# Kernel tuning notes

Hardware: AMD Instinct MI355X
Metric: run time of the kernel (lower is better)

Reference implementation:

```python
import jax, jax.numpy as jnp
import numpy as np

B, C, E, T, K = 8, 256, 512, 8192, 512
BN_EPS = 1e-5
UN_EPS = 1e-8


def setup_inputs() -> dict:
    key = jax.random.key(0)
    ks = jax.random.split(key, 6)
    sc_up = 1.0 / np.sqrt(C)
    sc_lin = 1.0 / np.sqrt(E)
    return {
        "x": jax.random.normal(ks[0], (B, C, T), jnp.float32),
        "up_w": jax.random.normal(ks[1], (E, C), jnp.float32) * sc_up,
        "up_b": jnp.zeros((E,), jnp.float32),
        "mask_w": jax.random.normal(ks[2], (E, C), jnp.float32) * sc_up,
        "mask_b": jnp.zeros((E,), jnp.float32),
        "sum_w": jax.random.normal(ks[3], (C, E), jnp.float32) * sc_lin,
        "sum_b": jnp.zeros((C,), jnp.float32),
        "down_w": jax.random.normal(ks[4], (C, E), jnp.float32) * sc_lin,
        "down_b": jnp.zeros((C,), jnp.float32),
        "bn_w": jnp.ones((C,), jnp.float32),
        "bn_b": jnp.zeros((C,), jnp.float32),
    }


def reference(x, up_w, up_b, mask_w, mask_b, sum_w, sum_b, down_w, down_b, bn_w, bn_b):
    b = x.shape[0]
    orig = x
    # 1x1 conv = channel matmul: (E,C) x (b,C,T) -> (b,E,T)
    up = jnp.einsum("ec,bct->bet", up_w, x) + up_b[None, :, None]
    # unit_norm over channel dim
    un = orig / (jnp.linalg.norm(orig, axis=1, keepdims=True) + UN_EPS)
    m = jnp.einsum("ec,bct->bet", mask_w, un) + mask_b[None, :, None]
    # softmax over flattened (E*T) per batch
    sm = jax.nn.softmax(m.reshape(b, -1), axis=-1)
    # sparsify: keep top-K softmax values per batch, zero the rest
    vals, idx = jax.lax.top_k(sm, K)  # (b,K)
    sp = jnp.zeros_like(sm).at[jnp.arange(b)[:, None], idx].set(vals)
    sp = sp.reshape(up.shape)
    gated = sp * up  # (b,E,T)
    summary = jnp.sum(gated, axis=-1)  # (b,E)
    proj = summary @ sum_w.T + sum_b  # (b,C)
    down = jnp.einsum("ce,bet->bct", down_w, gated) + down_b[None, :, None]
    y = down + proj[:, :, None]
    # BatchNorm1d (training mode: batch statistics, biased variance)
    mean = jnp.mean(y, axis=(0, 2), keepdims=True)
    var = jnp.var(y, axis=(0, 2), keepdims=True)
    out = (y - mean) / jnp.sqrt(var + BN_EPS) * bn_w[None, :, None] + bn_b[None, :, None]
    return out
```

## Files before the change

### kernel.cpp

```cpp
#include <hip/hip_runtime.h>
#include <hip/hip_bf16.h>

#define B_ 8
#define C_ 256
#define E_ 512
#define T_ 8192
#define K_ 512
#define CT_ (C_*T_)
#define BCAP_ 512
#define OCAP_ 1024
#define NBLK_ 2048
#define SUBS_ 64
#define SCOLS_ (T_/SUBS_)
#define SUBN_ (E_*SCOLS_)
#define RANK_ 64
#define NB1_ 4096
#define NB2_ 4096
#define TAUP_ 8
#define TAUM_ 0.004f

typedef __attribute__((ext_vector_type(8))) short bf16x8;
typedef __attribute__((ext_vector_type(4))) float f32x4;

__device__ __forceinline__ ushort f2bf(float f) {
    __hip_bfloat16 h = __float2bfloat16(f);
    return *reinterpret_cast<ushort*>(&h);
}
__device__ __forceinline__ float bf2f(ushort u) {
    __hip_bfloat16 h = *reinterpret_cast<__hip_bfloat16*>(&u);
    return __bfloat162float(h);
}

__device__ __forceinline__ void gl16(const void* g, void* l) {
    __builtin_amdgcn_global_load_lds(
        (const __attribute__((address_space(1))) void*)g,
        (__attribute__((address_space(3))) void*)l, 16, 0, 0);
}


__launch_bounds__(256)
__global__ void k_rn(const float* __restrict__ x, float* __restrict__ rn,
                     float* __restrict__ nrm, int* __restrict__ ovc,
                     int* __restrict__ map, float* __restrict__ spk) {
    __shared__ float partial[4][64];
    int tid = threadIdx.x, lane = tid & 63, w = tid >> 6;
    int bid = blockIdx.x;
    int gid = bid * 256 + tid;
    if (gid < B_) ovc[gid] = 0;
    if (gid < B_ * T_) map[gid] = -1;
    ((float4*)spk)[gid] = (float4){0.f, 0.f, 0.f, 0.f};
    int b = bid >> 7;
    int t = (bid & 127) * 64 + lane;
    const float* xp = x + (size_t)b * CT_ + (size_t)(w * 64) * T_ + t;
    float s0 = 0.f, s1 = 0.f, s2 = 0.f, s3 = 0.f;
#pragma unroll 4
    for (int c = 0; c < 64; c += 4) {
        float a0 = xp[(size_t)c * T_];
        float a1 = xp[(size_t)(c + 1) * T_];
        float a2 = xp[(size_t)(c + 2) * T_];
        float a3 = xp[(size_t)(c + 3) * T_];
        s0 += a0 * a0; s1 += a1 * a1; s2 += a2 * a2; s3 += a3 * a3;
    }
    partial[w][lane] = (s0 + s1) + (s2 + s3);
    __syncthreads();
    if (w == 0) {
        float s = (partial[0][lane] + partial[1][lane])
                + (partial[2][lane] + partial[3][lane]);
        float n = sqrtf(s) + 1e-8f;
        nrm[b * T_ + t] = n;
        rn[b * T_ + t] = 1.0f / n;
    }
}

__global__ void k_split_w(const float* __restrict__ mw, ushort* __restrict__ mwh,
                          ushort* __restrict__ mwl) {
    int idx = blockIdx.x * 256 + threadIdx.x;
    int erow = idx & 63;
    int cb = (idx >> 6) & 7;
    int cc = (idx >> 9) & 3;
    int etile = idx >> 11;
    int e = etile * 64 + erow;
    int c0 = cc * 64 + cb * 8;
    const float* src = mw + (size_t)e * C_ + c0;
    ushort4 h0, l0, h1, l1;
    float v;
    v = src[0]; h0.x = f2bf(v); l0.x = f2bf(v - bf2f(h0.x));
    v = src[1]; h0.y = f2bf(v); l0.y = f2bf(v - bf2f(h0.y));
    v = src[2]; h0.z = f2bf(v); l0.z = f2bf(v - bf2f(h0.z));
    v = src[3]; h0.w = f2bf(v); l0.w = f2bf(v - bf2f(h0.w));
    v = src[4]; h1.x = f2bf(v); l1.x = f2bf(v - bf2f(h1.x));
    v = src[5]; h1.y = f2bf(v); l1.y = f2bf(v - bf2f(h1.y));
    v = src[6]; h1.z = f2bf(v); l1.z = f2bf(v - bf2f(h1.z));
    v = src[7]; h1.w = f2bf(v); l1.w = f2bf(v - bf2f(h1.w));
    *(ushort4*)(mwh + (size_t)idx * 8) = h0;
    *(ushort4*)(mwh + (size_t)idx * 8 + 4) = h1;
    *(ushort4*)(mwl + (size_t)idx * 8) = l0;
    *(ushort4*)(mwl + (size_t)idx * 8 + 4) = l1;
}

__launch_bounds__(256)
__global__ void k_split_x(const float* __restrict__ x, const float* __restrict__ rn,
                          ushort* __restrict__ xh, ushort* __restrict__ xl) {
    __shared__ float tile[64][76];
    __shared__ float rnv[64];
    int tid = threadIdx.x;
    int ttile = blockIdx.x, cc = blockIdx.y, b = blockIdx.z;
    int t0 = ttile * 64, c0 = cc * 64;
    if (tid < 64) rnv[tid] = rn[b * T_ + t0 + tid];
    const float* xb = x + (size_t)b * CT_;
#pragma unroll
    for (int q = 0; q < 4; ++q) {
        int idx = tid + q * 256;
        int cr = idx >> 4, t4 = (idx & 15) * 4;
        float4 v = *(const float4*)(xb + (size_t)(c0 + cr) * T_ + t0 + t4);
        *(float4*)&tile[cr][t4] = v;
    }
    __syncthreads();
    size_t obase = (((size_t)b * 128 + ttile) * 4 + cc) * 4096;
#pragma unroll
    for (int q = 0; q < 4; ++q) {
        int idx = tid + q * 256;
        int tr = idx >> 4, c4 = (idx & 15) * 4;
        float s = rnv[tr];
        float v0 = tile[c4 + 0][tr] * s;
        float v1 = tile[c4 + 1][tr] * s;
        float v2 = tile[c4 + 2][tr] * s;
        float v3 = tile[c4 + 3][tr] * s;
        ushort4 h, l;
        h.x = f2bf(v0); l.x = f2bf(v0 - bf2f(h.x));
        h.y = f2bf(v1); l.y = f2bf(v1 - bf2f(h.y));
        h.z = f2bf(v2); l.z = f2bf(v2 - bf2f(h.z));
        h.w = f2bf(v3); l.w = f2bf(v3 - bf2f(h.w));
        int cb = c4 >> 3, half = (c4 >> 2) & 1;
        size_t ro = obase + (size_t)cb * 512 + tr * 8 + half * 4;
        *(ushort4*)(xh + ro) = h;
        *(ushort4*)(xl + ro) = l;
    }
}

__global__ void k_gather(const float* __restrict__ x, const float* __restrict__ rn,
                         float* __restrict__ xs, int* __restrict__ gh) {
    int gid = blockIdx.x * 256 + threadIdx.x;
    if (gid < B_ * NB1_) gh[gid] = 0;
    int s = gid & (SCOLS_ - 1);
    int c = (gid >> 7) & (C_ - 1);
    int b = gid >> 15;
    int t = s * SUBS_;
    xs[gid] = x[(size_t)b * CT_ + (size_t)c * T_ + t] * rn[b * T_ + t];
}

__launch_bounds__(256)
__global__ void k_msub2(const float* __restrict__ xs, const float* __restrict__ mw,
                        const float* __restrict__ mb, float* __restrict__ msub) {
    __shared__ float As[64][68];
    __shared__ float Bs[64][68];
    int tid = threadIdx.x;
    int tx = tid & 15, ty = tid >> 4;
    int s0 = blockIdx.x * 64, e0 = blockIdx.y * 64, b = blockIdx.z;
    const float* xb = xs + (size_t)b * C_ * SCOLS_;
    float acc[4][4] = {};
    for (int c0 = 0; c0 < C_; c0 += 64) {
#pragma unroll
        for (int r = 0; r < 4; ++r) {
            int i = (tid >> 4) + r * 16;
            int kq = (tid & 15) * 4;
            float4 av = *(const float4*)(mw + (size_t)(e0 + i) * C_ + c0 + kq);
            As[kq + 0][i] = av.x; As[kq + 1][i] = av.y;
            As[kq + 2][i] = av.z; As[kq + 3][i] = av.w;
        }
#pragma unroll
        for (int r = 0; r < 4; ++r) {
            int k = (tid >> 4) + r * 16;
            int jq = (tid & 15) * 4;
            *(float4*)(&Bs[k][jq]) =
                *(const float4*)(xb + (size_t)(c0 + k) * SCOLS_ + s0 + jq);
        }
        __syncthreads();
#pragma unroll
        for (int k = 0; k < 64; ++k) {
            float4 a = *(const float4*)(&As[k][ty * 4]);
            float4 bq = *(const float4*)(&Bs[k][tx * 4]);
            float av[4] = {a.x, a.y, a.z, a.w};
            float bv[4] = {bq.x, bq.y, bq.z, bq.w};
#pragma unroll
            for (int ii = 0; ii < 4; ++ii)
#pragma unroll
                for (int jj = 0; jj < 4; ++jj)
                    acc[ii][jj] += av[ii] * bv[jj];
        }
        __syncthreads();
    }
#pragma unroll
    for (int ii = 0; ii < 4; ++ii) {
        float mbv = mb[e0 + ty * 4 + ii];
#pragma unroll
        for (int jj = 0; jj < 4; ++jj) {
            int e = e0 + ty * 4 + ii, s = s0 + tx * 4 + jj;
            msub[(size_t)b * SUBN_ + e * SCOLS_ + s] = acc[ii][jj] + mbv;
        }
    }
}

__launch_bounds__(256)
__global__ void k_tau_hist(const float* __restrict__ msub, int* __restrict__ gh) {
    __shared__ int h[NB1_];
    int tid = threadIdx.x;
    int b = blockIdx.x >> 3, part = blockIdx.x & (TAUP_ - 1);
    for (int i = tid; i < NB1_; i += 256) h[i] = 0;
    __syncthreads();
    const float* mp = msub + (size_t)b * SUBN_ + part * (SUBN_ / TAUP_);
    for (int j = tid; j < SUBN_ / TAUP_; j += 256) {
        float v = mp[j];
        int bin = (int)((v + 1.0f) * ((float)NB1_ * 0.5f));
        bin = bin < 0 ? 0 : (bin > NB1_ - 1 ? NB1_ - 1 : bin);
        atomicAdd(&h[bin], 1);
    }
    __syncthreads();
    int* ghb = gh + b * NB1_;
    for (int i = tid; i < NB1_; i += 256)
        if (h[i]) atomicAdd(&ghb[i], h[i]);
}

__global__ void k_tau2(const int* __restrict__ gh, float* __restrict__ tau0) {
    __shared__ int part[256];
    int b = blockIdx.x, tid = threadIdx.x;
    const int* h = gh + b * NB1_;
    int ps = 0;
    for (int j = 0; j < 16; ++j) ps += h[tid * 16 + j];
    part[tid] = ps;
    __syncthreads();
    if (tid == 0) {
        int cum = 0, bf = 0;
        for (int i = 255; i >= 0; --i) {
            if (cum + part[i] >= RANK_) {
                int cum2 = cum;
                for (int j = 15; j >= 0; --j) {
                    cum2 += h[i * 16 + j];
                    if (cum2 >= RANK_) { bf = i * 16 + j; break; }
                }
                break;
            }
            cum += part[i];
        }
        tau0[b] = (float)bf * (2.0f / (float)NB1_) - 1.0f;
    }
}

__launch_bounds__(256)
__global__ void k_gemm128(const ushort* __restrict__ mwh, const ushort* __restrict__ xh,
                          const float* __restrict__ mb, const float* __restrict__ tau0,
                          float* __restrict__ zpart, int* __restrict__ cntB,
                          float* __restrict__ cvalB, int* __restrict__ cidxB,
                          int* __restrict__ ovc, float* __restrict__ ovv,
                          int* __restrict__ ovi) {
    __shared__ ushort S[4][4096];
    __shared__ float red[4];
    __shared__ float sval[BCAP_];
    __shared__ int sidx[BCAP_];
    __shared__ int scnt;
    int tid = threadIdx.x, lane = tid & 63, w = tid >> 6;
    int f = blockIdx.x;
    int xcd = f & 7, slot = f >> 3;
    int eblk = slot & 3, xt = slot >> 2;
    int xtile = xcd * 64 + xt;
    int b = xtile >> 6, tt = xtile & 63;
    int e0 = eblk * 128, t0 = tt * 128;
    if (tid == 0) scnt = 0;

    const ushort* base;
    if (w < 2) base = mwh + (size_t)(eblk * 2 + (w & 1)) * 16384;
    else       base = xh + ((size_t)b * 128 + tt * 2 + (w & 1)) * 16384;
    const ushort* gsrc = base + lane * 8;

    f32x4 acc[4][4];
#pragma unroll
    for (int m = 0; m < 4; ++m)
#pragma unroll
        for (int n = 0; n < 4; ++n)
            acc[m][n] = (f32x4){0.f, 0.f, 0.f, 0.f};

    int a15 = lane & 15;
    int khalf = lane >> 4;
    int wr = w >> 1, wc = w & 1;

    for (int cc = 0; cc < 4; ++cc) {
#pragma unroll
        for (int i = 0; i < 8; ++i)
            gl16(gsrc + cc * 4096 + i * 512, &S[w][0] + i * 512);
        __syncthreads();
#pragma unroll
        for (int ks = 0; ks < 2; ++ks) {
            int cb16 = ks * 4 + khalf;
            bf16x8 ah[4], bh[4];
#pragma unroll
            for (int m = 0; m < 4; ++m) {
                int aoff = (cb16 * 64 + m * 16 + a15) * 16;
                ah[m] = *(const bf16x8*)((const char*)&S[wr][0] + aoff);
            }
#pragma unroll
            for (int n = 0; n < 4; ++n) {
                int boff = (cb16 * 64 + n * 16 + a15) * 16;
                bh[n] = *(const bf16x8*)((const char*)&S[2 + wc][0] + boff);
            }
#pragma unroll
            for (int m = 0; m < 4; ++m)
#pragma unroll
                for (int n = 0; n < 4; ++n)
                    acc[m][n] = __builtin_amdgcn_mfma_f32_16x16x32_bf16(ah[m], bh[n], acc[m][n], 0, 0, 0);
        }
        __syncthreads();
    }

    float tau = tau0[b] - TAUM_;
    float zs = 0.f;
    int erow0 = e0 + wr * 64 + (lane >> 4) * 4;
#pragma unroll
    for (int m = 0; m < 4; ++m)
#pragma unroll
        for (int r = 0; r < 4; ++r) {
            int e = erow0 + m * 16 + r;
            float mbe = mb[e];
#pragma unroll
            for (int n = 0; n < 4; ++n) {
                int t = t0 + wc * 64 + n * 16 + a15;
                float v = acc[m][n][r] + mbe;
                zs += __expf(v);
                if (v >= tau) {
                    int pos = atomicAdd(&scnt, 1);
                    if (pos < BCAP_) {
                        sval[pos] = v;
                        sidx[pos] = e * T_ + t;
                    } else {
                        int q2 = atomicAdd(&ovc[b], 1);
                        if (q2 < OCAP_) {
                            ovv[b * OCAP_ + q2] = v;
                            ovi[b * OCAP_ + q2] = e * T_ + t;
                        }
                    }
                }
            }
        }
#pragma unroll
    for (int off = 32; off; off >>= 1) zs += __shfl_xor(zs, off, 64);
    if (lane == 0) red[w] = zs;
    __syncthreads();
    int nc = scnt < BCAP_ ? scnt : BCAP_;
    for (int j = tid; j < nc; j += 256) {
        cvalB[(size_t)f * BCAP_ + j] = sval[j];
        cidxB[(size_t)f * BCAP_ + j] = sidx[j];
    }
    if (tid == 0) {
        cntB[f] = nc;
        zpart[f] = (red[0] + red[1]) + (red[2] + red[3]);
    }
}

__launch_bounds__(256)
__global__ void k_exact(const ushort* __restrict__ mwh, const ushort* __restrict__ mwl,
                        const ushort* __restrict__ xh, const ushort* __restrict__ xl,
                        const float* __restrict__ mb, const int* __restrict__ cntB,
                        const int* __restrict__ cidxB, float* __restrict__ cvalB,
                        const int* __restrict__ ovc, const int* __restrict__ ovi,
                        float* __restrict__ ovv) {
    int f = blockIdx.x;
    int wv = threadIdx.x >> 6, lane = threadIdx.x & 63;
    int cc = lane >> 4, cb = (lane >> 1) & 7, half = lane & 1;
    int n, b;
    const int* ip;
    float* vp;
    if (f < NBLK_) {
        b = f & 7;
        n = cntB[f]; if (n > BCAP_) n = BCAP_;
        ip = cidxB + (size_t)f * BCAP_;
        vp = cvalB + (size_t)f * BCAP_;
    } else {
        b = f - NBLK_;
        n = ovc[b]; if (n > OCAP_) n = OCAP_;
        ip = ovi + (size_t)b * OCAP_;
        vp = ovv + (size_t)b * OCAP_;
    }
    for (int j = wv; j < n; j += 4) {
        int idx = ip[j];
        int e = idx >> 13, t = idx & (T_ - 1);
        size_t xro = ((((size_t)b * 128 + (t >> 6)) * 4 + cc) * 8 + cb) * 512
                   + (size_t)(t & 63) * 8 + half * 4;
        size_t wro = (((size_t)(e >> 6) * 4 + cc) * 8 + cb) * 512
                   + (size_t)(e & 63) * 8 + half * 4;
        ushort4 hx = *(const ushort4*)(xh + xro);
        ushort4 lx = *(const ushort4*)(xl + xro);
        ushort4 hw = *(const ushort4*)(mwh + wro);
        ushort4 lw = *(const ushort4*)(mwl + wro);
        float a = (bf2f(hw.x) + bf2f(lw.x)) * (bf2f(hx.x) + bf2f(lx.x))
                + (bf2f(hw.y) + bf2f(lw.y)) * (bf2f(hx.y) + bf2f(lx.y))
                + (bf2f(hw.z) + bf2f(lw.z)) * (bf2f(hx.z) + bf2f(lx.z))
                + (bf2f(hw.w) + bf2f(lw.w)) * (bf2f(hx.w) + bf2f(lx.w));
#pragma unroll
        for (int off = 32; off; off >>= 1) a += __shfl_xor(a, off, 64);
        if (lane == 0) vp[j] = a + mb[e];
    }
}

__launch_bounds__(1024)
__global__ void k_selectc(const float* __restrict__ zpart, const int* __restrict__ cntB,
                          const float* __restrict__ cvalB, const int* __restrict__ cidxB,
                          const int* __restrict__ ovc, const float* __restrict__ ovv,
                          const int* __restrict__ ovi, int* __restrict__ sel_e,
                          int* __restrict__ sel_t, float* __restrict__ sel_sp) {
    __shared__ float zsh[256];
    __shared__ int h[NB2_];
    __shared__ int part[256];
    __shared__ float bl_v[1024];
    __shared__ int bl_i[1024];
    __shared__ int nb, bstar, nabove, outcnt;
    int b = blockIdx.x, tid = threadIdx.x;
    int rid = tid & 255, sub = tid >> 8;
    int f = b + 8 * rid;
    int c = cntB[f];
    for (int i = tid; i < NB2_; i += 1024) h[i] = 0;
    if (tid < 256) zsh[tid] = zpart[b + 8 * tid];
    if (tid == 0) { nb = 0; outcnt = 0; bstar = 0; nabove = 0; }
    __syncthreads();
    const float* rv = cvalB + (size_t)f * BCAP_;
    for (int j = sub; j < c; j += 4) {
        float v = rv[j];
        int bin = (int)(v * ((float)NB2_ * 2.0f));
        bin = bin < 0 ? 0 : (bin > NB2_ - 1 ? NB2_ - 1 : bin);
        atomicAdd(&h[bin], 1);
    }
    int no = ovc[b]; if (no > OCAP_) no = OCAP_;
    for (int j = tid; j < no; j += 1024) {
        float v = ovv[b * OCAP_ + j];
        int bin = (int)(v * ((float)NB2_ * 2.0f));
        bin = bin < 0 ? 0 : (bin > NB2_ - 1 ? NB2_ - 1 : bin);
        atomicAdd(&h[bin], 1);
    }
    __syncthreads();
    for (int d = 128; d; d >>= 1) {
        if (tid < d) zsh[tid] += zsh[tid + d];
        __syncthreads();
    }
    if (tid < 256) {
        int ps = 0;
#pragma unroll
        for (int j = 0; j < 16; ++j) ps += h[tid * 16 + j];
        part[tid] = ps;
    }
    __syncthreads();
    for (int d = 1; d < 256; d <<= 1) {
        int v = 0;
        if (tid < 256) v = (tid + d < 256) ? part[tid + d] : 0;
        __syncthreads();
        if (tid < 256) part[tid] += v;
        __syncthreads();
    }
    if (tid < 256 && part[tid] >= K_ && (tid == 255 || part[tid + 1] < K_)) {
        int cum2 = (tid == 255) ? 0 : part[tid + 1];
        for (int j = 15; j >= 0; --j) {
            cum2 += h[tid * 16 + j];
            if (cum2 >= K_) { bstar = tid * 16 + j; nabove = cum2 - h[tid * 16 + j]; break; }
        }
    }
    __syncthreads();
    int bs = bstar;
    float rZ = 1.0f / zsh[0];
    const int* ri = cidxB + (size_t)f * BCAP_;
    for (int j = sub; j < c; j += 4) {
        float v = rv[j];
        int bin = (int)(v * ((float)NB2_ * 2.0f));
        bin = bin < 0 ? 0 : (bin > NB2_ - 1 ? NB2_ - 1 : bin);
        if (bin > bs) {
            int q = atomicAdd(&outcnt, 1);
            int idx = ri[j];
            sel_e[b * K_ + q] = idx / T_;
            sel_t[b * K_ + q] = idx % T_;
            sel_sp[b * K_ + q] = __expf(v) * rZ;
        } else if (bin == bs) {
            int q = atomicAdd(&nb, 1);
            if (q < 1024) { bl_v[q] = v; bl_i[q] = ri[j]; }
        }
    }
    for (int j = tid; j < no; j += 1024) {
        float v = ovv[b * OCAP_ + j];
        int bin = (int)(v * ((float)NB2_ * 2.0f));
        bin = bin < 0 ? 0 : (bin > NB2_ - 1 ? NB2_ - 1 : bin);
        if (bin > bs) {
            int q = atomicAdd(&outcnt, 1);
            int idx = ovi[b * OCAP_ + j];
            sel_e[b * K_ + q] = idx / T_;
            sel_t[b * K_ + q] = idx % T_;
            sel_sp[b * K_ + q] = __expf(v) * rZ;
        } else if (bin == bs) {
            int q = atomicAdd(&nb, 1);
            if (q < 1024) { bl_v[q] = v; bl_i[q] = ovi[b * OCAP_ + j]; }
        }
    }
    __syncthreads();
    int m = nb; if (m > 1024) m = 1024;
    int need = K_ - nabove;
    for (int j = tid; j < m; j += 1024) {
        float v = bl_v[j]; int id = bl_i[j];
        int r = 0;
        for (int i = 0; i < m; ++i) {
            float vi = bl_v[i]; int ii = bl_i[i];
            r += (vi > v || (vi == v && ii < id)) ? 1 : 0;
        }
        if (r < need) {
            int slot = nabove + r;
            sel_e[b * K_ + slot] = id / T_;
            sel_t[b * K_ + slot] = id % T_;
            sel_sp[b * K_ + slot] = __expf(v) * rZ;
        }
    }
    for (int q = m + tid; q < need; q += 1024) {
        int slot = nabove + q;
        sel_e[b * K_ + slot] = 0; sel_t[b * K_ + slot] = 0;
        sel_sp[b * K_ + slot] = 0.f;
    }
}

__global__ void k_upg2(const ushort* __restrict__ xh, const ushort* __restrict__ xl,
                       const float* __restrict__ nrm, const float* __restrict__ uw,
                       const float* __restrict__ ub, const int* __restrict__ sel_e,
                       const int* __restrict__ sel_t, const float* __restrict__ sel_sp,
                       float* __restrict__ gval) {
    int gid = blockIdx.x * 256 + threadIdx.x;
    int w = gid >> 6, lane = gid & 63;
    int b = w >> 9, i = w & (K_ - 1);
    int e = sel_e[b * K_ + i], t = sel_t[b * K_ + i];
    int ttile = t >> 6, trow = t & 63;
    int cc = lane >> 4, cb = (lane >> 1) & 7, half = lane & 1;
    size_t ro = ((((size_t)b * 128 + ttile) * 4 + cc) * 8 + cb) * 512
              + (size_t)trow * 8 + half * 4;
    ushort4 h = *(const ushort4*)(xh + ro);
    ushort4 l = *(const ushort4*)(xl + ro);
    float4 wv = *(const float4*)(uw + (size_t)e * C_ + lane * 4);
    float acc = (bf2f(h.x) + bf2f(l.x)) * wv.x + (bf2f(h.y) + bf2f(l.y)) * wv.y
              + (bf2f(h.z) + bf2f(l.z)) * wv.z + (bf2f(h.w) + bf2f(l.w)) * wv.w;
#pragma unroll
    for (int off = 32; off; off >>= 1) acc += __shfl_down(acc, off, 64);
    if (lane == 0)
        gval[b * K_ + i] = sel_sp[b * K_ + i] * (acc * nrm[b * T_ + t] + ub[e]);
}

__launch_bounds__(256)
__global__ void k_bsqbn(const float* __restrict__ sw, const float* __restrict__ sb,
                        const float* __restrict__ db, const float* __restrict__ dw,
                        const int* __restrict__ sel_e, const float* __restrict__ gval,
                        const float* __restrict__ bnw, const float* __restrict__ bnb,
                        float* __restrict__ scalec, float* __restrict__ obase) {
    __shared__ float barr[8], s1arr[8], qarr[8];
    int c = blockIdx.x;
    int w = threadIdx.x >> 6, lane = threadIdx.x & 63;
#pragma unroll
    for (int rep = 0; rep < 2; ++rep) {
        int b = w + rep * 4;
        float p = 0.f, s = 0.f, q = 0.f;
        for (int i = lane; i < K_; i += 64) {
            int e = sel_e[b * K_ + i];
            float g = gval[b * K_ + i];
            p += g * sw[(size_t)c * E_ + e];
            float wv = dw[(size_t)c * E_ + e] * g;
            s += wv; q += wv * wv;
        }
#pragma unroll
        for (int off = 32; off; off >>= 1) {
            p += __shfl_xor(p, off, 64);
            s += __shfl_xor(s, off, 64);
            q += __shfl_xor(q, off, 64);
        }
        if (lane == 0) {
            barr[b] = p + sb[c] + db[c];
            s1arr[b] = s; qarr[b] = q;
        }
    }
    __syncthreads();
    if (threadIdx.x == 0) {
        float msum = 0.f;
        for (int b = 0; b < B_; ++b) msum += (float)T_ * barr[b] + s1arr[b];
        float mean = msum / (float)(B_ * T_);
        float vs = 0.f;
        for (int b = 0; b < B_; ++b) {
            float d = barr[b] - mean;
            vs += (float)T_ * d * d + 2.0f * d * s1arr[b] + qarr[b];
        }
        float var = vs / (float)(B_ * T_);
        float sc = bnw[c] * rsqrtf(var + 1e-5f);
        scalec[c] = sc;
        for (int b = 0; b < B_; ++b)
            obase[b * C_ + c] = (barr[b] - mean) * sc + bnb[c];
    }
}

__global__ void k_spk1(const int* __restrict__ sel_t, int* __restrict__ map,
                       int* __restrict__ pri) {
    int gid = blockIdx.x * 256 + threadIdx.x;
    int b = gid >> 9;
    int t = sel_t[gid];
    int old = atomicCAS(&map[b * T_ + t], -1, gid & (K_ - 1));
    pri[gid] = (old == -1) ? (gid & (K_ - 1)) : old;
}

__global__ void k_spk2(const float* __restrict__ dw, const float* __restrict__ scalec,
                       const int* __restrict__ sel_e, const int* __restrict__ pri,
                       const float* __restrict__ gval, float* __restrict__ spk) {
    int gid = blockIdx.x * 256 + threadIdx.x;
    int s = gid >> 6, cq = (gid & 63) * 4;
    int b = s >> 9;
    int e = sel_e[s];
    float g = gval[s];
    int p = pri[s];
    float* dst = spk + ((size_t)(b * K_ + p)) * C_ + cq;
#pragma unroll
    for (int q = 0; q < 4; ++q) {
        int c = cq + q;
        atomicAdd(dst + q, scalec[c] * dw[(size_t)c * E_ + e] * g);
    }
}

__global__ void k_fill2(const float* __restrict__ obase, const int* __restrict__ map,
                        const float* __restrict__ spk, float* __restrict__ out) {
    size_t gid = (size_t)blockIdx.x * 256 + threadIdx.x;
    size_t flat = gid * 4;
    int b = (int)(flat / CT_);
    int c = (int)(flat / T_) & (C_ - 1);
    int t0 = (int)(flat & (T_ - 1));
    float v = obase[b * C_ + c];
    float4 o = {v, v, v, v};
    int4 mp = *(const int4*)(map + b * T_ + t0);
    if (mp.x >= 0) o.x += spk[((size_t)(b * K_ + mp.x)) * C_ + c];
    if (mp.y >= 0) o.y += spk[((size_t)(b * K_ + mp.y)) * C_ + c];
    if (mp.z >= 0) o.z += spk[((size_t)(b * K_ + mp.z)) * C_ + c];
    if (mp.w >= 0) o.w += spk[((size_t)(b * K_ + mp.w)) * C_ + c];
    *(float4*)(out + flat) = o;
}

extern "C" void kernel_launch(void* const* d_in, const int* in_sizes, int n_in,
                              void* d_out, int out_size, void* d_ws, size_t ws_size,
                              hipStream_t stream) {
    const float* x = (const float*)d_in[0];
    const float* up_w = (const float*)d_in[1];
    const float* up_b = (const float*)d_in[2];
    const float* mask_w = (const float*)d_in[3];
    const float* mask_b = (const float*)d_in[4];
    const float* sum_w = (const float*)d_in[5];
    const float* sum_b = (const float*)d_in[6];
    const float* down_w = (const float*)d_in[7];
    const float* down_b = (const float*)d_in[8];
    const float* bn_w = (const float*)d_in[9];
    const float* bn_b = (const float*)d_in[10];
    float* out = (float*)d_out;

    float* ws = (float*)d_ws;
    size_t o = 0;
    float* rn = ws + o;   o += (size_t)B_ * T_;
    float* nrm = ws + o;  o += (size_t)B_ * T_;
    float* xs = ws + o;   o += (size_t)B_ * C_ * SCOLS_;
    float* msub = ws + o; o += (size_t)B_ * SUBN_;
    float* tau0 = ws + o; o += B_;
    int* gh = (int*)(ws + o);    o += (size_t)B_ * NB1_;
    int* sel_e = (int*)(ws + o); o += (size_t)B_ * K_;
    int* sel_t = (int*)(ws + o); o += (size_t)B_ * K_;
    float* sel_sp = ws + o; o += (size_t)B_ * K_;
    float* gval = ws + o;   o += (size_t)B_ * K_;
    float* scalec = ws + o; o += C_;
    float* obase = ws + o;  o += (size_t)B_ * C_ + 8;
    float* zpart = ws + o;  o += NBLK_;
    int* cntB = (int*)(ws + o); o += NBLK_;
    float* cvalB = ws + o;  o += (size_t)NBLK_ * BCAP_;
    int* cidxB = (int*)(ws + o); o += (size_t)NBLK_ * BCAP_;
    int* ovc = (int*)(ws + o); o += B_;
    float* ovv = ws + o;    o += (size_t)B_ * OCAP_;
    int* ovi = (int*)(ws + o); o += (size_t)B_ * OCAP_;
    int* map = (int*)(ws + o);  o += (size_t)B_ * T_;
    int* pri = (int*)(ws + o);  o += (size_t)B_ * K_;
    float* spk = ws + o;        o += (size_t)B_ * K_ * C_;
    ushort* mwh = (ushort*)(ws + o); o += (size_t)E_ * C_ / 2;
    ushort* mwl = (ushort*)(ws + o); o += (size_t)E_ * C_ / 2;
    ushort* xh = (ushort*)(ws + o);  o += (size_t)B_ * T_ * C_ / 2;
    ushort* xl = (ushort*)(ws + o);  o += (size_t)B_ * T_ * C_ / 2;
    (void)ws_size;

    k_rn<<<(B_ * T_) / 64, 256, 0, stream>>>(x, rn, nrm, ovc, map, spk);
    k_gather<<<(B_ * C_ * SCOLS_) / 256, 256, 0, stream>>>(x, rn, xs, gh);
    k_msub2<<<dim3(SCOLS_ / 64, E_ / 64, B_), 256, 0, stream>>>(xs, mask_w, mask_b, msub);
    k_tau_hist<<<B_ * TAUP_, 256, 0, stream>>>(msub, gh);
    k_tau2<<<B_, 256, 0, stream>>>(gh, tau0);
    k_split_w<<<(E_ * C_ / 8) / 256, 256, 0, stream>>>(mask_w, mwh, mwl);
    k_split_x<<<dim3(T_ / 64, C_ / 64, B_), 256, 0, stream>>>(x, rn, xh, xl);
    k_gemm128<<<NBLK_, 256, 0, stream>>>(mwh, xh, mask_b, tau0,
                                         zpart, cntB, cvalB, cidxB,
                                         ovc, ovv, ovi);
    k_exact<<<NBLK_ + B_, 256, 0, stream>>>(mwh, mwl, xh, xl, mask_b,
                                            cntB, cidxB, cvalB, ovc, ovi, ovv);
    k_selectc<<<B_, 1024, 0, stream>>>(zpart, cntB, cvalB, cidxB,
                                       ovc, ovv, ovi, sel_e, sel_t, sel_sp);
    k_spk1<<<(B_ * K_) / 256, 256, 0, stream>>>(sel_t, map, pri);
    k_upg2<<<(B_ * K_ * 64) / 256, 256, 0, stream>>>(xh, xl, nrm, up_w, up_b,
                                                     sel_e, sel_t, sel_sp, gval);
    k_bsqbn<<<C_, 256, 0, stream>>>(sum_w, sum_b, down_b, down_w, sel_e, gval,
                                    bn_w, bn_b, scalec, obase);
    k_spk2<<<(B_ * K_ * 64) / 256, 256, 0, stream>>>(down_w, scalec, sel_e, pri,
                                                     gval, spk);
    k_fill2<<<(B_ * CT_ / 4) / 256, 256, 0, stream>>>(obase, map, spk, out);
}
```

Baseline: 212.2 us.

## Fold gather, weight split and spk1 kernels into neighbouring kernels

```diff
diff --git a/kernel.cpp b/kernel.cpp
--- a/kernel.cpp
+++ b/kernel.cpp
@@ -41,16 +41,21 @@
 __launch_bounds__(256)
 __global__ void k_rn(const float* __restrict__ x, float* __restrict__ rn,
                      float* __restrict__ nrm, int* __restrict__ ovc,
-                     int* __restrict__ map, float* __restrict__ spk) {
+                     int* __restrict__ map, float* __restrict__ spk,
+                     float* __restrict__ xs, int* __restrict__ gh) {
     __shared__ float partial[4][64];
+    __shared__ float xcol[256];
+    __shared__ float rn0;
     int tid = threadIdx.x, lane = tid & 63, w = tid >> 6;
     int bid = blockIdx.x;
     int gid = bid * 256 + tid;
     if (gid < B_) ovc[gid] = 0;
     if (gid < B_ * T_) map[gid] = -1;
+    if (gid < B_ * NB1_) gh[gid] = 0;
     ((float4*)spk)[gid] = (float4){0.f, 0.f, 0.f, 0.f};
     int b = bid >> 7;
-    int t = (bid & 127) * 64 + lane;
+    int s = bid & 127;
+    int t = s * 64 + lane;
     const float* xp = x + (size_t)b * CT_ + (size_t)(w * 64) * T_ + t;
     float s0 = 0.f, s1 = 0.f, s2 = 0.f, s3 = 0.f;
 #pragma unroll 4
@@ -59,48 +64,34 @@
         float a1 = xp[(size_t)(c + 1) * T_];
         float a2 = xp[(size_t)(c + 2) * T_];
         float a3 = xp[(size_t)(c + 3) * T_];
+        if (lane == 0) {
+            xcol[w * 64 + c] = a0;
+            xcol[w * 64 + c + 1] = a1;
+            xcol[w * 64 + c + 2] = a2;
+            xcol[w * 64 + c + 3] = a3;
+        }
         s0 += a0 * a0; s1 += a1 * a1; s2 += a2 * a2; s3 += a3 * a3;
     }
     partial[w][lane] = (s0 + s1) + (s2 + s3);
     __syncthreads();
     if (w == 0) {
-        float s = (partial[0][lane] + partial[1][lane])
-                + (partial[2][lane] + partial[3][lane]);
-        float n = sqrtf(s) + 1e-8f;
+        float sx = (partial[0][lane] + partial[1][lane])
+                 + (partial[2][lane] + partial[3][lane]);
+        float n = sqrtf(sx) + 1e-8f;
         nrm[b * T_ + t] = n;
-        rn[b * T_ + t] = 1.0f / n;
-    }
-}
-
-__global__ void k_split_w(const float* __restrict__ mw, ushort* __restrict__ mwh,
-                          ushort* __restrict__ mwl) {
-    int idx = blockIdx.x * 256 + threadIdx.x;
-    int erow = idx & 63;
-    int cb = (idx >> 6) & 7;
-    int cc = (idx >> 9) & 3;
-    int etile = idx >> 11;
-    int e = etile * 64 + erow;
-    int c0 = cc * 64 + cb * 8;
-    const float* src = mw + (size_t)e * C_ + c0;
-    ushort4 h0, l0, h1, l1;
-    float v;
-    v = src[0]; h0.x = f2bf(v); l0.x = f2bf(v - bf2f(h0.x));
-    v = src[1]; h0.y = f2bf(v); l0.y = f2bf(v - bf2f(h0.y));
-    v = src[2]; h0.z = f2bf(v); l0.z = f2bf(v - bf2f(h0.z));
-    v = src[3]; h0.w = f2bf(v); l0.w = f2bf(v - bf2f(h0.w));
-    v = src[4]; h1.x = f2bf(v); l1.x = f2bf(v - bf2f(h1.x));
-    v = src[5]; h1.y = f2bf(v); l1.y = f2bf(v - bf2f(h1.y));
-    v = src[6]; h1.z = f2bf(v); l1.z = f2bf(v - bf2f(h1.z));
-    v = src[7]; h1.w = f2bf(v); l1.w = f2bf(v - bf2f(h1.w));
-    *(ushort4*)(mwh + (size_t)idx * 8) = h0;
-    *(ushort4*)(mwh + (size_t)idx * 8 + 4) = h1;
-    *(ushort4*)(mwl + (size_t)idx * 8) = l0;
-    *(ushort4*)(mwl + (size_t)idx * 8 + 4) = l1;
+        float r = 1.0f / n;
+        rn[b * T_ + t] = r;
+        if (lane == 0) rn0 = r;
+    }
+    __syncthreads();
+    xs[b * (C_ * SCOLS_) + tid * SCOLS_ + s] = xcol[tid] * rn0;
 }
 
 __launch_bounds__(256)
 __global__ void k_split_x(const float* __restrict__ x, const float* __restrict__ rn,
-                          ushort* __restrict__ xh, ushort* __restrict__ xl) {
+                          ushort* __restrict__ xh, ushort* __restrict__ xl,
+                          const float* __restrict__ mw, ushort* __restrict__ mwh,
+                          ushort* __restrict__ mwl) {
     __shared__ float tile[64][76];
     __shared__ float rnv[64];
     int tid = threadIdx.x;
@@ -121,11 +112,11 @@
     for (int q = 0; q < 4; ++q) {
         int idx = tid + q * 256;
         int tr = idx >> 4, c4 = (idx & 15) * 4;
-        float s = rnv[tr];
-        float v0 = tile[c4 + 0][tr] * s;
-        float v1 = tile[c4 + 1][tr] * s;
-        float v2 = tile[c4 + 2][tr] * s;
-        float v3 = tile[c4 + 3][tr] * s;
+        float sc = rnv[tr];
+        float v0 = tile[c4 + 0][tr] * sc;
+        float v1 = tile[c4 + 1][tr] * sc;
+        float v2 = tile[c4 + 2][tr] * sc;
+        float v3 = tile[c4 + 3][tr] * sc;
         ushort4 h, l;
         h.x = f2bf(v0); l.x = f2bf(v0 - bf2f(h.x));
         h.y = f2bf(v1); l.y = f2bf(v1 - bf2f(h.y));
@@ -136,17 +127,32 @@
         *(ushort4*)(xh + ro) = h;
         *(ushort4*)(xl + ro) = l;
     }
-}
-
-__global__ void k_gather(const float* __restrict__ x, const float* __restrict__ rn,
-                         float* __restrict__ xs, int* __restrict__ gh) {
-    int gid = blockIdx.x * 256 + threadIdx.x;
-    if (gid < B_ * NB1_) gh[gid] = 0;
-    int s = gid & (SCOLS_ - 1);
-    int c = (gid >> 7) & (C_ - 1);
-    int b = gid >> 15;
-    int t = s * SUBS_;
-    xs[gid] = x[(size_t)b * CT_ + (size_t)c * T_ + t] * rn[b * T_ + t];
+    if (ttile == 0 && cc == 0) {
+        for (int r = 0; r < 8; ++r) {
+            int idx = b * 2048 + r * 256 + tid;
+            int erow = idx & 63;
+            int cbw = (idx >> 6) & 7;
+            int ccw = (idx >> 9) & 3;
+            int etile = idx >> 11;
+            int e = etile * 64 + erow;
+            int c0w = ccw * 64 + cbw * 8;
+            const float* src = mw + (size_t)e * C_ + c0w;
+            ushort4 h0, l0, h1, l1;
+            float v;
+            v = src[0]; h0.x = f2bf(v); l0.x = f2bf(v - bf2f(h0.x));
+            v = src[1]; h0.y = f2bf(v); l0.y = f2bf(v - bf2f(h0.y));
+            v = src[2]; h0.z = f2bf(v); l0.z = f2bf(v - bf2f(h0.z));
+            v = src[3]; h0.w = f2bf(v); l0.w = f2bf(v - bf2f(h0.w));
+            v = src[4]; h1.x = f2bf(v); l1.x = f2bf(v - bf2f(h1.x));
+            v = src[5]; h1.y = f2bf(v); l1.y = f2bf(v - bf2f(h1.y));
+            v = src[6]; h1.z = f2bf(v); l1.z = f2bf(v - bf2f(h1.z));
+            v = src[7]; h1.w = f2bf(v); l1.w = f2bf(v - bf2f(h1.w));
+            *(ushort4*)(mwh + (size_t)idx * 8) = h0;
+            *(ushort4*)(mwh + (size_t)idx * 8 + 4) = h1;
+            *(ushort4*)(mwl + (size_t)idx * 8) = l0;
+            *(ushort4*)(mwl + (size_t)idx * 8 + 4) = l1;
+        }
+    }
 }
 
 __launch_bounds__(256)
@@ -522,11 +528,16 @@
                        const float* __restrict__ nrm, const float* __restrict__ uw,
                        const float* __restrict__ ub, const int* __restrict__ sel_e,
                        const int* __restrict__ sel_t, const float* __restrict__ sel_sp,
-                       float* __restrict__ gval) {
+                       float* __restrict__ gval, int* __restrict__ map,
+                       int* __restrict__ pri) {
     int gid = blockIdx.x * 256 + threadIdx.x;
     int w = gid >> 6, lane = gid & 63;
     int b = w >> 9, i = w & (K_ - 1);
     int e = sel_e[b * K_ + i], t = sel_t[b * K_ + i];
+    if (lane == 0) {
+        int old = atomicCAS(&map[b * T_ + t], -1, i);
+        pri[b * K_ + i] = (old == -1) ? i : old;
+    }
     int ttile = t >> 6, trow = t & 63;
     int cc = lane >> 4, cb = (lane >> 1) & 7, half = lane & 1;
     size_t ro = ((((size_t)b * 128 + ttile) * 4 + cc) * 8 + cb) * 512
@@ -589,15 +600,6 @@
         for (int b = 0; b < B_; ++b)
             obase[b * C_ + c] = (barr[b] - mean) * sc + bnb[c];
     }
-}
-
-__global__ void k_spk1(const int* __restrict__ sel_t, int* __restrict__ map,
-                       int* __restrict__ pri) {
-    int gid = blockIdx.x * 256 + threadIdx.x;
-    int b = gid >> 9;
-    int t = sel_t[gid];
-    int old = atomicCAS(&map[b * T_ + t], -1, gid & (K_ - 1));
-    pri[gid] = (old == -1) ? (gid & (K_ - 1)) : old;
 }
 
 __global__ void k_spk2(const float* __restrict__ dw, const float* __restrict__ scalec,
@@ -680,13 +682,12 @@
     ushort* xl = (ushort*)(ws + o);  o += (size_t)B_ * T_ * C_ / 2;
     (void)ws_size;
 
-    k_rn<<<(B_ * T_) / 64, 256, 0, stream>>>(x, rn, nrm, ovc, map, spk);
-    k_gather<<<(B_ * C_ * SCOLS_) / 256, 256, 0, stream>>>(x, rn, xs, gh);
+    k_rn<<<(B_ * T_) / 64, 256, 0, stream>>>(x, rn, nrm, ovc, map, spk, xs, gh);
     k_msub2<<<dim3(SCOLS_ / 64, E_ / 64, B_), 256, 0, stream>>>(xs, mask_w, mask_b, msub);
     k_tau_hist<<<B_ * TAUP_, 256, 0, stream>>>(msub, gh);
     k_tau2<<<B_, 256, 0, stream>>>(gh, tau0);
-    k_split_w<<<(E_ * C_ / 8) / 256, 256, 0, stream>>>(mask_w, mwh, mwl);
-    k_split_x<<<dim3(T_ / 64, C_ / 64, B_), 256, 0, stream>>>(x, rn, xh, xl);
+    k_split_x<<<dim3(T_ / 64, C_ / 64, B_), 256, 0, stream>>>(x, rn, xh, xl,
+                                                              mask_w, mwh, mwl);
     k_gemm128<<<NBLK_, 256, 0, stream>>>(mwh, xh, mask_b, tau0,
                                          zpart, cntB, cvalB, cidxB,
                                          ovc, ovv, ovi);
@@ -694,9 +695,9 @@
                                             cntB, cidxB, cvalB, ovc, ovi, ovv);
     k_selectc<<<B_, 1024, 0, stream>>>(zpart, cntB, cvalB, cidxB,
                                        ovc, ovv, ovi, sel_e, sel_t, sel_sp);
-    k_spk1<<<(B_ * K_) / 256, 256, 0, stream>>>(sel_t, map, pri);
     k_upg2<<<(B_ * K_ * 64) / 256, 256, 0, stream>>>(xh, xl, nrm, up_w, up_b,
-                                                     sel_e, sel_t, sel_sp, gval);
+                                                     sel_e, sel_t, sel_sp, gval,
+                                                     map, pri);
     k_bsqbn<<<C_, 256, 0, stream>>>(sum_w, sum_b, down_b, down_w, sel_e, gval,
                                     bn_w, bn_b, scalec, obase);
     k_spk2<<<(B_ * K_ * 64) / 256, 256, 0, stream>>>(down_w, scalec, sel_e, pri,
```

New measurement: 209.9 us. No clear change (-1.1%).
